# Kernel optimization log

Hardware: AMD Instinct MI355X
Metric: run time of the kernel (lower is better)

Reference implementation:

```python
import jax, jax.numpy as jnp
import numpy as np

DMODEL = 1024
NHEAD = 16
DHEAD = DMODEL // NHEAD

def _layernorm(x, g, b, eps=1e-5):
    mu = jnp.mean(x, axis=-1, keepdims=True)
    var = jnp.var(x, axis=-1, keepdims=True)
    return (x - mu) * jax.lax.rsqrt(var + eps) * g + b

def setup_inputs() -> dict:
    key = jax.random.key(0)
    ks = jax.random.split(key, 12)
    b, lq, lv, d = 2, 2048, 2048, DMODEL
    s = 1.0 / np.sqrt(d)
    return {
        "q": jax.random.normal(ks[0], (b, lq, d), jnp.float32),
        "k": jax.random.normal(ks[1], (b, lv, d), jnp.float32),
        "v": jax.random.normal(ks[2], (b, lv, d), jnp.float32),
        "qln_g": jnp.ones((d,), jnp.float32),
        "qln_b": jnp.zeros((d,), jnp.float32),
        "kvln_g": jnp.ones((d,), jnp.float32),
        "kvln_b": jnp.zeros((d,), jnp.float32),
        "Wq": jax.random.normal(ks[3], (d, d), jnp.float32) * s,
        "Wk": jax.random.normal(ks[4], (d, d), jnp.float32) * s,
        "Wv": jax.random.normal(ks[5], (d, d), jnp.float32) * s,
        "Wg": jax.random.normal(ks[6], (d, d), jnp.float32) * s,
        "bg": jnp.zeros((d,), jnp.float32),
        "Wo": jax.random.normal(ks[7], (d, d), jnp.float32) * s,
    }

def reference(q, k, v, qln_g, qln_b, kvln_g, kvln_b, Wq, Wk, Wv, Wg, bg, Wo):
    b, lq, d = q.shape
    lv = v.shape[1]
    qn = _layernorm(q, qln_g, qln_b)           # [b, lq, d]
    q_ = qn @ Wq.T
    kk = _layernorm(k, kvln_g, kvln_b) @ Wk.T
    vv = _layernorm(v, kvln_g, kvln_b) @ Wv.T
    qh = q_.reshape(b, lq, NHEAD, DHEAD)       # bqhd
    kh = kk.reshape(b, lv, NHEAD, DHEAD)
    vh = vv.reshape(b, lv, NHEAD, DHEAD)
    scores = jnp.einsum('bqhd,bkhd->bhqk', qh, kh) / np.sqrt(DHEAD)
    attn = jax.nn.softmax(scores, axis=-1)
    y = jnp.einsum('bhqk,bkhd->bqhd', attn, vh).reshape(b, lq, d)
    g = jax.nn.sigmoid(qn @ Wg.T + bg)
    return (y * g) @ Wo.T
```

## Files before the change

### kernel.cpp

```cpp
#include <hip/hip_runtime.h>
#include <hip/hip_bf16.h>

#define DMODEL 1024
#define NHEAD  16
#define DHEAD  64
#define BATCH  2
#define LQ     2048
#define LV     2048
#define ROWS   (BATCH*LQ)
#define WELEMS (DMODEL*DMODEL)
#define BH     (BATCH*NHEAD)

typedef short bf16x8 __attribute__((ext_vector_type(8)));
typedef float f32x4  __attribute__((ext_vector_type(4)));

__device__ __forceinline__ float bf2f(unsigned short s) {
    union { unsigned u; float f; } v; v.u = ((unsigned)s) << 16;
    return v.f;
}
__device__ __forceinline__ unsigned pk_bf(float a, float b) {
    union { __hip_bfloat162 h; unsigned u; } c;
    c.h = __float22bfloat162_rn(make_float2(a, b));
    return c.u;
}

__device__ __forceinline__ void cp16_g2l(const void* g, void* l) {
    __builtin_amdgcn_global_load_lds(
        (const __attribute__((address_space(1))) void*)g,
        (__attribute__((address_space(3))) void*)l,
        16, 0, 0);
}

#define QSCALE (0.125f * 1.4426950408889634f)

__global__ __launch_bounds__(256) void prep_kernel(
    const float* q, const float* k, const float* v,
    const float* qg, const float* qb, const float* kvg, const float* kvb,
    const float* Wq, const float* Wk, const float* Wv, const float* Wg, const float* Wo,
    unsigned short* qn, unsigned short* kn, unsigned short* vn, unsigned short* wb)
{
    __shared__ float rs[4], rq[4];
    int z = blockIdx.y;
    if (z < 5) {
        if (blockIdx.x >= WELEMS / 1024) return;
        const float* srcs[5] = {Wq, Wk, Wv, Wg, Wo};
        const float* s = srcs[z];
        unsigned short* d = wb + (size_t)z * WELEMS;
        int i = (blockIdx.x * 256 + threadIdx.x) * 4;
        float4 x = *(const float4*)(s + i);
        uint2 o = make_uint2(pk_bf(x.x, x.y), pk_bf(x.z, x.w));
        *(uint2*)(d + i) = o;
        return;
    }
    int row = blockIdx.x;
    const float *x, *gp, *bp; unsigned short* o;
    if      (z == 5) { x = q; gp = qg;  bp = qb;  o = qn; }
    else if (z == 6) { x = k; gp = kvg; bp = kvb; o = kn; }
    else             { x = v; gp = kvg; bp = kvb; o = vn; }

    int col = threadIdx.x * 4;
    float4 xv = *(const float4*)(x + (size_t)row * DMODEL + col);
    float s  = xv.x + xv.y + xv.z + xv.w;
    float sq = xv.x*xv.x + xv.y*xv.y + xv.z*xv.z + xv.w*xv.w;
    #pragma unroll
    for (int off = 1; off < 64; off <<= 1) { s += __shfl_xor(s, off); sq += __shfl_xor(sq, off); }

    int wave = threadIdx.x >> 6, lane = threadIdx.x & 63;
    if (lane == 0) { rs[wave] = s; rq[wave] = sq; }
    __syncthreads();
    float ts = rs[0] + rs[1] + rs[2] + rs[3];
    float tq = rq[0] + rq[1] + rq[2] + rq[3];
    float mu  = ts * (1.0f / DMODEL);
    float var = tq * (1.0f / DMODEL) - mu * mu;
    float inv = rsqrtf(var + 1e-5f);

    float4 gv = *(const float4*)(gp + col);
    float4 bv = *(const float4*)(bp + col);
    float r0 = (xv.x - mu) * inv * gv.x + bv.x;
    float r1 = (xv.y - mu) * inv * gv.y + bv.y;
    float r2 = (xv.z - mu) * inv * gv.z + bv.z;
    float r3 = (xv.w - mu) * inv * gv.w + bv.w;
    *(uint2*)(o + (size_t)row * DMODEL + col) = make_uint2(pk_bf(r0, r1), pk_bf(r2, r3));
}

template<int MODE>
__device__ __forceinline__ void gemm_bt_core(
    const unsigned short* A, const unsigned short* Bw,
    unsigned short* Obf, float* Of32, const float* bias, float scale,
    unsigned short* Al, unsigned short* Bl, int bm, int bn)
{
    int tid  = threadIdx.x;
    int wave = tid >> 6, lane = tid & 63, quad = lane >> 4, L = lane & 15;
    int wm = wave >> 1, wn = wave & 1;

    int srow = wave * 16 + (lane >> 2);
    int scol = (lane & 3) * 8;
    const unsigned short* gA = A  + (size_t)(bm * 128 + srow) * DMODEL + scol;
    const unsigned short* gB = Bw + (size_t)(bn * 128 + srow) * DMODEL + scol;
    int lofs0 = wave * 16 * 32;
    int lofs1 = (64 + wave * 16) * 32;

    f32x4 acc[4][4];
    #pragma unroll
    for (int i = 0; i < 4; ++i)
        #pragma unroll
        for (int j = 0; j < 4; ++j) acc[i][j] = (f32x4){0.f, 0.f, 0.f, 0.f};

    cp16_g2l(gA,               Al + lofs0);
    cp16_g2l(gA + 64 * DMODEL, Al + lofs1);
    cp16_g2l(gB,               Bl + lofs0);
    cp16_g2l(gB + 64 * DMODEL, Bl + lofs1);

    int buf = 0;
    for (int k0 = 0; k0 < DMODEL; k0 += 32, buf ^= 1) {
        __syncthreads();
        if (k0 + 32 < DMODEL) {
            int nb = (buf ^ 1) * (128 * 32);
            cp16_g2l(gA + k0 + 32,               Al + nb + lofs0);
            cp16_g2l(gA + 64 * DMODEL + k0 + 32, Al + nb + lofs1);
            cp16_g2l(gB + k0 + 32,               Bl + nb + lofs0);
            cp16_g2l(gB + 64 * DMODEL + k0 + 32, Bl + nb + lofs1);
        }
        const unsigned short* Ab = Al + buf * (128 * 32);
        const unsigned short* Bb = Bl + buf * (128 * 32);
        bf16x8 af[4], bfr[4];
        #pragma unroll
        for (int i = 0; i < 4; ++i)
            af[i] = *(const bf16x8*)&Ab[(wm * 64 + i * 16 + L) * 32 + quad * 8];
        #pragma unroll
        for (int j = 0; j < 4; ++j)
            bfr[j] = *(const bf16x8*)&Bb[(wn * 64 + j * 16 + L) * 32 + quad * 8];
        #pragma unroll
        for (int i = 0; i < 4; ++i)
            #pragma unroll
            for (int j = 0; j < 4; ++j) {
                if (MODE == 3)
                    acc[i][j] = __builtin_amdgcn_mfma_f32_16x16x32_bf16(af[i], bfr[j], acc[i][j], 0, 0, 0);
                else
                    acc[i][j] = __builtin_amdgcn_mfma_f32_16x16x32_bf16(bfr[j], af[i], acc[i][j], 0, 0, 0);
            }
    }

    #pragma unroll
    for (int i = 0; i < 4; ++i) {
        #pragma unroll
        for (int j = 0; j < 4; ++j) {
            f32x4 a = acc[i][j];
            if (MODE == 3) {
                int gcol  = bn * 128 + wn * 64 + j * 16 + L;
                int grow0 = bm * 128 + wm * 64 + i * 16 + quad * 4;
                int b = grow0 >> 11, key0 = grow0 & 2047;
                int h = gcol >> 6,   dd   = gcol & 63;
                uint2 o = make_uint2(pk_bf(a[0], a[1]), pk_bf(a[2], a[3]));
                *(uint2*)&Obf[(((size_t)(b * NHEAD + h) * DHEAD + dd) << 11) + key0] = o;
            } else {
                int grow  = bm * 128 + wm * 64 + i * 16 + L;
                int gcol0 = bn * 128 + wn * 64 + j * 16 + quad * 4;
                size_t idx = (size_t)grow * DMODEL + gcol0;
                if (MODE == 0) {
                    uint2 o = make_uint2(pk_bf(a[0] * scale, a[1] * scale),
                                         pk_bf(a[2] * scale, a[3] * scale));
                    *(uint2*)&Obf[idx] = o;
                } else if (MODE == 1) {
                    float4 bv = *(const float4*)&bias[gcol0];
                    float s0 = 1.0f / (1.0f + __expf(-(a[0] + bv.x)));
                    float s1 = 1.0f / (1.0f + __expf(-(a[1] + bv.y)));
                    float s2 = 1.0f / (1.0f + __expf(-(a[2] + bv.z)));
                    float s3 = 1.0f / (1.0f + __expf(-(a[3] + bv.w)));
                    *(uint2*)&Obf[idx] = make_uint2(pk_bf(s0, s1), pk_bf(s2, s3));
                } else {
                    *(f32x4*)&Of32[idx] = a;
                }
            }
        }
    }
}

__device__ __forceinline__ void xcd_map(int& bm, int& bn) {
    int f = blockIdx.y * 8 + blockIdx.x;
    int xcd = f & 7, s = f >> 3;
    bn = s & 7;
    bm = ((s >> 3) << 3) | xcd;
}

__global__ __launch_bounds__(256) void gemm_batched_kernel(
    const unsigned short* qn, const unsigned short* kn, const unsigned short* vn,
    const unsigned short* wb,
    unsigned short* qs, unsigned short* kkp, unsigned short* vt, unsigned short* gate,
    const float* bg)
{
    __shared__ __align__(16) unsigned short Al[2 * 128 * 32];
    __shared__ __align__(16) unsigned short Bl[2 * 128 * 32];
    int bm, bn; xcd_map(bm, bn);
    switch (blockIdx.z) {
        case 0:  gemm_bt_core<0>(qn, wb + 0 * WELEMS, qs,   nullptr, nullptr, QSCALE, Al, Bl, bm, bn); break;
        case 1:  gemm_bt_core<0>(kn, wb + 1 * WELEMS, kkp,  nullptr, nullptr, 1.0f,   Al, Bl, bm, bn); break;
        case 2:  gemm_bt_core<3>(vn, wb + 2 * WELEMS, vt,   nullptr, nullptr, 1.0f,   Al, Bl, bm, bn); break;
        default: gemm_bt_core<1>(qn, wb + 3 * WELEMS, gate, nullptr, bg,      1.0f,   Al, Bl, bm, bn); break;
    }
}

__global__ __launch_bounds__(256) void gemm_f32out_kernel(
    const unsigned short* A, const unsigned short* Bw, float* O)
{
    __shared__ __align__(16) unsigned short Al[2 * 128 * 32];
    __shared__ __align__(16) unsigned short Bl[2 * 128 * 32];
    int bm, bn; xcd_map(bm, bn);
    gemm_bt_core<2>(A, Bw, nullptr, O, nullptr, 1.0f, Al, Bl, bm, bn);
}

#define ASTR 72

__global__ __launch_bounds__(256, 5) void attn_kernel(
    const unsigned short* qs, const unsigned short* kk, const unsigned short* vt,
    const unsigned short* gate, unsigned short* yg)
{
    __shared__ __align__(16) unsigned short Kl[64 * ASTR];
    __shared__ __align__(16) unsigned short Vl[64 * ASTR];
    __shared__ __align__(16) unsigned short Pl[64 * ASTR];

    int tid  = threadIdx.x;
    int wave = tid >> 6, lane = tid & 63, quad = lane >> 4, L = lane & 15;

    int f  = blockIdx.y * 32 + blockIdx.x;
    int bh = (f & 7) * 4 + ((f >> 3) & 3);
    int qt = f >> 5;
    int bb = bh >> 4, h = bh & 15;
    int q0 = qt * 64;

    const unsigned short* Qb =
        qs + ((size_t)(bb * LQ + q0 + wave * 16 + L)) * DMODEL + h * DHEAD;
    bf16x8 aq0 = *(const bf16x8*)(Qb + quad * 8);
    bf16x8 aq1 = *(const bf16x8*)(Qb + 32 + quad * 8);

    f32x4 acc[4];
    #pragma unroll
    for (int nt = 0; nt < 4; ++nt) acc[nt] = (f32x4){0.f, 0.f, 0.f, 0.f};
    f32x4 lacc = (f32x4){0.f, 0.f, 0.f, 0.f};
    bf16x8 ones;
    #pragma unroll
    for (int j = 0; j < 8; ++j) ones[j] = (short)0x3F80;

    unsigned short* Pw = &Pl[wave * 16 * ASTR];
    int r0 = tid >> 3, c0 = (tid & 7) * 8;

    const unsigned short* Kg = kk + ((size_t)bb * LV) * DMODEL + h * DHEAD;
    const unsigned short* Vg = vt + ((size_t)(bb * NHEAD + h) * DHEAD) * LV;

    for (int it = 0; it < LV / 64; ++it) {
        int kv0 = it * 64;
        __syncthreads();
        *(uint4*)&Kl[r0 * ASTR + c0]        = *(const uint4*)&Kg[(size_t)(kv0 + r0) * DMODEL + c0];
        *(uint4*)&Kl[(r0 + 32) * ASTR + c0] = *(const uint4*)&Kg[(size_t)(kv0 + r0 + 32) * DMODEL + c0];
        *(uint4*)&Vl[r0 * ASTR + c0]        = *(const uint4*)&Vg[(size_t)r0 * LV + kv0 + c0];
        *(uint4*)&Vl[(r0 + 32) * ASTR + c0] = *(const uint4*)&Vg[(size_t)(r0 + 32) * LV + kv0 + c0];
        __syncthreads();

        #pragma unroll
        for (int kt = 0; kt < 4; ++kt) {
            bf16x8 bk0 = *(const bf16x8*)&Kl[(kt * 16 + L) * ASTR + quad * 8];
            bf16x8 bk1 = *(const bf16x8*)&Kl[(kt * 16 + L) * ASTR + 32 + quad * 8];
            f32x4 z = (f32x4){0.f, 0.f, 0.f, 0.f};
            z = __builtin_amdgcn_mfma_f32_16x16x32_bf16(bk0, aq0, z, 0, 0, 0);
            z = __builtin_amdgcn_mfma_f32_16x16x32_bf16(bk1, aq1, z, 0, 0, 0);
            uint2 pk2 = make_uint2(pk_bf(exp2f(z[0]), exp2f(z[1])),
                                   pk_bf(exp2f(z[2]), exp2f(z[3])));
            *(uint2*)&Pw[L * ASTR + kt * 16 + quad * 4] = pk2;
        }

        asm volatile("s_waitcnt lgkmcnt(0)" ::: "memory");

        bf16x8 pa0 = *(const bf16x8*)&Pw[L * ASTR + quad * 8];
        bf16x8 pa1 = *(const bf16x8*)&Pw[L * ASTR + 32 + quad * 8];
        lacc = __builtin_amdgcn_mfma_f32_16x16x32_bf16(ones, pa0, lacc, 0, 0, 0);
        lacc = __builtin_amdgcn_mfma_f32_16x16x32_bf16(ones, pa1, lacc, 0, 0, 0);
        #pragma unroll
        for (int nt = 0; nt < 4; ++nt) {
            bf16x8 vb0 = *(const bf16x8*)&Vl[(nt * 16 + L) * ASTR + quad * 8];
            bf16x8 vb1 = *(const bf16x8*)&Vl[(nt * 16 + L) * ASTR + 32 + quad * 8];
            acc[nt] = __builtin_amdgcn_mfma_f32_16x16x32_bf16(vb0, pa0, acc[nt], 0, 0, 0);
            acc[nt] = __builtin_amdgcn_mfma_f32_16x16x32_bf16(vb1, pa1, acc[nt], 0, 0, 0);
        }
    }

    float inv_l = 1.0f / lacc[0];
    size_t rb = ((size_t)(bb * LQ + q0 + wave * 16 + L)) * DMODEL + h * DHEAD;
    #pragma unroll
    for (int nt = 0; nt < 4; ++nt) {
        size_t idx = rb + nt * 16 + quad * 4;
        ushort4 g = *(const ushort4*)&gate[idx];
        float y0 = acc[nt][0] * inv_l * bf2f(g.x);
        float y1 = acc[nt][1] * inv_l * bf2f(g.y);
        float y2 = acc[nt][2] * inv_l * bf2f(g.z);
        float y3 = acc[nt][3] * inv_l * bf2f(g.w);
        *(uint2*)&yg[idx] = make_uint2(pk_bf(y0, y1), pk_bf(y2, y3));
    }
}

extern "C" void kernel_launch(void* const* d_in, const int* in_sizes, int n_in,
                              void* d_out, int out_size, void* d_ws, size_t ws_size,
                              hipStream_t stream)
{
    const float* q      = (const float*)d_in[0];
    const float* k      = (const float*)d_in[1];
    const float* v      = (const float*)d_in[2];
    const float* qln_g  = (const float*)d_in[3];
    const float* qln_b  = (const float*)d_in[4];
    const float* kvln_g = (const float*)d_in[5];
    const float* kvln_b = (const float*)d_in[6];
    const float* Wq     = (const float*)d_in[7];
    const float* Wk     = (const float*)d_in[8];
    const float* Wv     = (const float*)d_in[9];
    const float* Wg     = (const float*)d_in[10];
    const float* bg     = (const float*)d_in[11];
    const float* Wo     = (const float*)d_in[12];
    float* out = (float*)d_out;

    const size_t T8 = (size_t)ROWS * DMODEL * 2;
    char* ws = (char*)d_ws;
    unsigned short* qn   = (unsigned short*)(ws + 0 * T8);
    unsigned short* kn   = (unsigned short*)(ws + 1 * T8);
    unsigned short* vn   = (unsigned short*)(ws + 2 * T8);
    unsigned short* qs   = (unsigned short*)(ws + 3 * T8);
    unsigned short* kkp  = (unsigned short*)(ws + 4 * T8);
    unsigned short* vt   = (unsigned short*)(ws + 5 * T8);
    unsigned short* gate = (unsigned short*)(ws + 6 * T8);
    unsigned short* yg   = (unsigned short*)(ws + 7 * T8);
    unsigned short* wb   = (unsigned short*)(ws + 8 * T8);

    prep_kernel<<<dim3(ROWS, 8), 256, 0, stream>>>(
        q, k, v, qln_g, qln_b, kvln_g, kvln_b, Wq, Wk, Wv, Wg, Wo, qn, kn, vn, wb);
    gemm_batched_kernel<<<dim3(DMODEL / 128, ROWS / 128, 4), 256, 0, stream>>>(
        qn, kn, vn, wb, qs, kkp, vt, gate, bg);
    attn_kernel<<<dim3(32, 32), 256, 0, stream>>>(qs, kkp, vt, gate, yg);
    gemm_f32out_kernel<<<dim3(DMODEL / 128, ROWS / 128), 256, 0, stream>>>(yg, wb + 4 * WELEMS, out);
}
```

Before: 268.6 us.

## Double-buffer attention K/V via async copies and keep P in registers

Rewrites the attention inner loop to prefetch the next K/V tile with direct global-to-LDS copies into a double buffer, so each iteration needs one barrier instead of two. K rows are permuted so the score MFMA output lands in the layout the PV MFMA needs, which keeps P in registers instead of staging it through shared memory. It also uses an XOR-swizzled LDS layout in place of padding, the raw exp2 intrinsic, and s_setprio around MFMA blocks. Occupancy hint drops from 5 to 4 blocks per CU, and the code relies on a cp16_g2l helper and a wait on the async copies before the barrier, neither of which is visible here.

```diff
diff --git a/kernel.cpp b/kernel.cpp
--- a/kernel.cpp
+++ b/kernel.cpp
@@ -209,15 +209,12 @@
     gemm_bt_core<2>(A, Bw, nullptr, O, nullptr, 1.0f, Al, Bl, bm, bn);
 }
 
-#define ASTR 72
-
-__global__ __launch_bounds__(256, 5) void attn_kernel(
+__global__ __launch_bounds__(256, 4) void attn_kernel(
     const unsigned short* qs, const unsigned short* kk, const unsigned short* vt,
     const unsigned short* gate, unsigned short* yg)
 {
-    __shared__ __align__(16) unsigned short Kl[64 * ASTR];
-    __shared__ __align__(16) unsigned short Vl[64 * ASTR];
-    __shared__ __align__(16) unsigned short Pl[64 * ASTR];
+    __shared__ __align__(16) unsigned short Kl[2 * 64 * 64];
+    __shared__ __align__(16) unsigned short Vl[2 * 64 * 64];
 
     int tid  = threadIdx.x;
     int wave = tid >> 6, lane = tid & 63, quad = lane >> 4, L = lane & 15;
@@ -241,46 +238,72 @@
     #pragma unroll
     for (int j = 0; j < 8; ++j) ones[j] = (short)0x3F80;
 
-    unsigned short* Pw = &Pl[wave * 16 * ASTR];
-    int r0 = tid >> 3, c0 = (tid & 7) * 8;
-
-    const unsigned short* Kg = kk + ((size_t)bb * LV) * DMODEL + h * DHEAD;
-    const unsigned short* Vg = vt + ((size_t)(bb * NHEAD + h) * DHEAD) * LV;
-
-    for (int it = 0; it < LV / 64; ++it) {
-        int kv0 = it * 64;
+    int rloc = lane >> 3;
+    int c16  = (lane & 7) ^ rloc;
+    int key0 = (wave & 1) * 32 + (rloc >> 2) * 8 + (wave >> 1) * 4 + (rloc & 3);
+
+    const unsigned short* gK = kk + (size_t)bb * LV * DMODEL + h * DHEAD
+                                  + (size_t)key0 * DMODEL + c16 * 8;
+    const unsigned short* gV = vt + ((size_t)((bb * NHEAD + h) * DHEAD
+                                  + wave * 16 + rloc)) * LV + c16 * 8;
+    char* KlB = (char*)Kl;
+    char* VlB = (char*)Vl;
+    int dst0 = wave * 2048;
+
+    cp16_g2l(gK,               KlB + dst0);
+    cp16_g2l(gK + 16 * DMODEL, KlB + dst0 + 1024);
+    cp16_g2l(gV,               VlB + dst0);
+    cp16_g2l(gV + 8 * LV,      VlB + dst0 + 1024);
+
+    int sl0 = (quad ^ (L & 7)) * 8;
+    int buf = 0;
+    for (int it = 0; it < LV / 64; ++it, buf ^= 1) {
         __syncthreads();
-        *(uint4*)&Kl[r0 * ASTR + c0]        = *(const uint4*)&Kg[(size_t)(kv0 + r0) * DMODEL + c0];
-        *(uint4*)&Kl[(r0 + 32) * ASTR + c0] = *(const uint4*)&Kg[(size_t)(kv0 + r0 + 32) * DMODEL + c0];
-        *(uint4*)&Vl[r0 * ASTR + c0]        = *(const uint4*)&Vg[(size_t)r0 * LV + kv0 + c0];
-        *(uint4*)&Vl[(r0 + 32) * ASTR + c0] = *(const uint4*)&Vg[(size_t)(r0 + 32) * LV + kv0 + c0];
-        __syncthreads();
-
+        if (it + 1 < LV / 64) {
+            gK += 64 * DMODEL; gV += 64;
+            int nb = (buf ^ 1) * 8192 + dst0;
+            cp16_g2l(gK,               KlB + nb);
+            cp16_g2l(gK + 16 * DMODEL, KlB + nb + 1024);
+            cp16_g2l(gV,               VlB + nb);
+            cp16_g2l(gV + 8 * LV,      VlB + nb + 1024);
+        }
+        const unsigned short* Kb = Kl + buf * 4096;
+        const unsigned short* Vb = Vl + buf * 4096;
+
+        f32x4 zz[4];
+        __builtin_amdgcn_s_setprio(1);
         #pragma unroll
         for (int kt = 0; kt < 4; ++kt) {
-            bf16x8 bk0 = *(const bf16x8*)&Kl[(kt * 16 + L) * ASTR + quad * 8];
-            bf16x8 bk1 = *(const bf16x8*)&Kl[(kt * 16 + L) * ASTR + 32 + quad * 8];
+            bf16x8 bk0 = *(const bf16x8*)&Kb[(kt * 16 + L) * 64 + sl0];
+            bf16x8 bk1 = *(const bf16x8*)&Kb[(kt * 16 + L) * 64 + (sl0 ^ 32)];
             f32x4 z = (f32x4){0.f, 0.f, 0.f, 0.f};
             z = __builtin_amdgcn_mfma_f32_16x16x32_bf16(bk0, aq0, z, 0, 0, 0);
             z = __builtin_amdgcn_mfma_f32_16x16x32_bf16(bk1, aq1, z, 0, 0, 0);
-            uint2 pk2 = make_uint2(pk_bf(exp2f(z[0]), exp2f(z[1])),
-                                   pk_bf(exp2f(z[2]), exp2f(z[3])));
-            *(uint2*)&Pw[L * ASTR + kt * 16 + quad * 4] = pk2;
-        }
-
-        asm volatile("s_waitcnt lgkmcnt(0)" ::: "memory");
-
-        bf16x8 pa0 = *(const bf16x8*)&Pw[L * ASTR + quad * 8];
-        bf16x8 pa1 = *(const bf16x8*)&Pw[L * ASTR + 32 + quad * 8];
-        lacc = __builtin_amdgcn_mfma_f32_16x16x32_bf16(ones, pa0, lacc, 0, 0, 0);
-        lacc = __builtin_amdgcn_mfma_f32_16x16x32_bf16(ones, pa1, lacc, 0, 0, 0);
+            zz[kt] = z;
+        }
+        __builtin_amdgcn_s_setprio(0);
+
+        union { unsigned u[4]; bf16x8 h; } pa0, pa1;
+        pa0.u[0] = pk_bf(__builtin_amdgcn_exp2f(zz[0][0]), __builtin_amdgcn_exp2f(zz[0][1]));
+        pa0.u[1] = pk_bf(__builtin_amdgcn_exp2f(zz[0][2]), __builtin_amdgcn_exp2f(zz[0][3]));
+        pa0.u[2] = pk_bf(__builtin_amdgcn_exp2f(zz[2][0]), __builtin_amdgcn_exp2f(zz[2][1]));
+        pa0.u[3] = pk_bf(__builtin_amdgcn_exp2f(zz[2][2]), __builtin_amdgcn_exp2f(zz[2][3]));
+        pa1.u[0] = pk_bf(__builtin_amdgcn_exp2f(zz[1][0]), __builtin_amdgcn_exp2f(zz[1][1]));
+        pa1.u[1] = pk_bf(__builtin_amdgcn_exp2f(zz[1][2]), __builtin_amdgcn_exp2f(zz[1][3]));
+        pa1.u[2] = pk_bf(__builtin_amdgcn_exp2f(zz[3][0]), __builtin_amdgcn_exp2f(zz[3][1]));
+        pa1.u[3] = pk_bf(__builtin_amdgcn_exp2f(zz[3][2]), __builtin_amdgcn_exp2f(zz[3][3]));
+
+        __builtin_amdgcn_s_setprio(1);
+        lacc = __builtin_amdgcn_mfma_f32_16x16x32_bf16(ones, pa0.h, lacc, 0, 0, 0);
+        lacc = __builtin_amdgcn_mfma_f32_16x16x32_bf16(ones, pa1.h, lacc, 0, 0, 0);
         #pragma unroll
         for (int nt = 0; nt < 4; ++nt) {
-            bf16x8 vb0 = *(const bf16x8*)&Vl[(nt * 16 + L) * ASTR + quad * 8];
-            bf16x8 vb1 = *(const bf16x8*)&Vl[(nt * 16 + L) * ASTR + 32 + quad * 8];
-            acc[nt] = __builtin_amdgcn_mfma_f32_16x16x32_bf16(vb0, pa0, acc[nt], 0, 0, 0);
-            acc[nt] = __builtin_amdgcn_mfma_f32_16x16x32_bf16(vb1, pa1, acc[nt], 0, 0, 0);
-        }
+            bf16x8 vb0 = *(const bf16x8*)&Vb[(nt * 16 + L) * 64 + sl0];
+            bf16x8 vb1 = *(const bf16x8*)&Vb[(nt * 16 + L) * 64 + (sl0 ^ 32)];
+            acc[nt] = __builtin_amdgcn_mfma_f32_16x16x32_bf16(vb0, pa0.h, acc[nt], 0, 0, 0);
+            acc[nt] = __builtin_amdgcn_mfma_f32_16x16x32_bf16(vb1, pa1.h, acc[nt], 0, 0, 0);
+        }
+        __builtin_amdgcn_s_setprio(0);
     }
 
     float inv_l = 1.0f / lacc[0];
```

Measured after the change: 249.2 us. 7.2% less time.
